# Performance work log

Measured on AMD Instinct MI355X. Metric: run time of the kernel, lower is better.

Reference implementation:

```python
import jax, jax.numpy as jnp
import numpy as np
from jax import lax

# ---- static config (from BasePllay_2 / AdTopoLayer(out_features=50, T=25, m0=0.2, lims=[[224,0],[0,224]], K_max=2, p=0)) ----
H = W = 28
G = H * W
T = 25
K_MAX = 2
M0 = 0.2
OUT_FEATURES = 50
B = 32
TSEQ = jnp.linspace(0.0, 100.0, T)  # fixed landscape sample grid (covers DTM value range)

# static grid geometry from lims=[[224,0],[0,224]]
_xs = np.linspace(224.0, 0.0, H)
_ys = np.linspace(0.0, 224.0, W)
_pts = np.stack(np.meshgrid(_xs, _ys, indexing="ij"), -1).reshape(G, 2)
_d = np.sqrt(((_pts[:, None] - _pts[None]) ** 2).sum(-1))
_sidx = np.argsort(_d, axis=-1)
SDIST = jnp.asarray(np.take_along_axis(_d, _sidx, -1), jnp.float32)  # [G,G] sorted distances per grid point
SIDX = jnp.asarray(_sidx.astype(np.int32))                            # [G,G] static distance-sort order

# 4-connectivity neighbor table for the cubical (pixel) grid, -1 = invalid
_ii = np.arange(G).reshape(H, W)
_nb = np.full((H, W, 4), -1, np.int32)
_nb[1:, :, 0] = _ii[:-1, :]
_nb[:-1, :, 1] = _ii[1:, :]
_nb[:, 1:, 2] = _ii[:, :-1]
_nb[:, :-1, 3] = _ii[:, 1:]
NBR = jnp.asarray(_nb.reshape(G, 4))


def dtm(w):
    """Weighted distance-to-measure (r=2) on the fixed grid. w: [B,G] nonneg -> [B,G]."""
    sw = w[:, SIDX]                               # [B,G,G] weights in distance order
    cw = jnp.cumsum(sw, -1)
    d2 = SDIST ** 2
    cwd = jnp.cumsum(sw * d2[None], -1)
    bound = M0 * w.sum(-1)                        # [B]
    k = jnp.argmax(cw >= bound[:, None, None], -1)  # [B,G] first index reaching mass bound
    km1 = jnp.maximum(k - 1, 0)
    take = lambda a, i: jnp.take_along_axis(a, i[..., None], -1)[..., 0]
    has_prev = k > 0
    cw_p = jnp.where(has_prev, take(cw, km1), 0.0)
    cwd_p = jnp.where(has_prev, take(cwd, km1), 0.0)
    dk2 = d2[jnp.arange(G)[None, :], k]           # [B,G]
    val = (cwd_p + (bound[:, None] - cw_p) * dk2) / bound[:, None]
    return jnp.sqrt(jnp.maximum(val, 0.0))


def pd0(vals):
    """0-dim sublevel-set persistence of vals on the pixel grid (union-find, elder rule).
    Returns (births[G], deaths[G]); non-merging pixels yield zero-persistence pairs,
    essential components die at the max filtration value."""
    order = jnp.argsort(vals).astype(jnp.int32)
    rank = jnp.zeros(G, jnp.int32).at[order].set(jnp.arange(G, dtype=jnp.int32))

    def find(parent, i):
        return lax.while_loop(lambda j: parent[j] != j, lambda j: parent[j], i)

    def step(s, carry):
        parent, death = carry
        p = order[s]
        best = p
        for t in range(4):  # unrolled over the 4 grid neighbors (static)
            q = NBR[p, t]
            ok = (q >= 0) & (rank[jnp.maximum(q, 0)] < s)  # neighbor already inserted
            r = find(parent, jnp.where(ok, q, p))
            merge = ok & (r != best)
            r_old = rank[r] < rank[best]
            older = jnp.where(r_old, r, best)
            younger = jnp.where(r_old, best, r)
            widx = jnp.where(merge, younger, G)   # slot G is a dummy
            parent = parent.at[widx].set(older)
            death = death.at[widx].set(p)         # younger component dies at pixel p
            best = jnp.where(merge, older, best)
        return parent, death

    parent0 = jnp.arange(G + 1, dtype=jnp.int32)
    death0 = jnp.full(G + 1, -1, jnp.int32)
    _, death = lax.fori_loop(0, G, step, (parent0, death0))
    d = death[:G]
    deaths = jnp.where(d >= 0, vals[jnp.maximum(d, 0)], vals.max())
    return vals, deaths


def landscape(births, deaths):
    """K_MAX persistence landscapes sampled at TSEQ. [B,G] -> [B, K_MAX*T]."""
    tb = TSEQ[None, :, None] - births[:, None, :]   # [B,T,G]
    td = deaths[:, None, :] - TSEQ[None, :, None]
    tent = jnp.maximum(jnp.minimum(tb, td), 0.0)
    topk = lax.top_k(tent, K_MAX)[0]                # [B,T,K]
    return jnp.transpose(topk, (0, 2, 1)).reshape(births.shape[0], K_MAX * T)


def _forward(x, w_land, b_land, w_fc, b_fc):
    w = x.reshape(x.shape[0], -1)          # nn.Flatten: pixel intensities as measure weights
    v = dtm(w)                             # [B,G]
    births, deaths = jax.vmap(pd0)(v)
    feats = landscape(births, deaths)      # [B, 50]
    xt = feats @ w_land.T + b_land         # AdTopoLayer output [B, out_features]
    signal = jnp.abs(lax.stop_gradient(xt)).sum(0)   # torch: x.detach().abs().sum(0)
    out = jnp.maximum(xt, 0.0) @ w_fc.T + b_fc       # fc(relu(x))
    return out, signal

_forward_jit = jax.jit(_forward)


def setup_inputs() -> dict:
    key = jax.random.key(0)
    k = jax.random.split(key, 4)
    x = jax.random.uniform(k[0], (B, 1, H, W), jnp.float32)  # image-like nonneg weights
    w_land = jax.random.normal(k[1], (OUT_FEATURES, K_MAX * T), jnp.float32) * 0.1
    b_land = jnp.zeros((OUT_FEATURES,), jnp.float32)
    w_fc = jax.random.normal(k[2], (10, OUT_FEATURES), jnp.float32) * 0.1
    b_fc = jnp.zeros((10,), jnp.float32)
    return {"x": x, "w_land": w_land, "b_land": b_land, "w_fc": w_fc, "b_fc": b_fc}


def reference(x, w_land, b_land, w_fc, b_fc):
    return _forward_jit(x, w_land, b_land, w_fc, b_fc)
```

## Files before the change

### kernel.cpp

```cpp
#include <hip/hip_runtime.h>
#include <math.h>

#define H28 28
#define G784 784
#define BATCH 32
#define NOFF 3025
#define NOFFP 3072
#define NKEY 1459
#define TPTS 25
#define KMAX 2
#define NFEAT 50
#define OUTF 50
#define NCLS 10

#define NBX 28
#define BT 512
#define BT2 512
#define HS 2048
#define EMAX 1024

struct OffPair { unsigned ij; float d2; };
struct OffTab  { OffPair e[NOFFP]; };

constexpr double csqrt(double x) {
  double r = x * 0.5 + 1.0;
  for (int i = 0; i < 20; i++) r = 0.5 * (r + x / r);
  return r;
}

constexpr OffTab make_offtab() {
  OffTab t{};
  int start[NKEY] = {};
  for (int i = 0; i < NOFF; i++) {
    int di = i / 55 - 27, dj = i % 55 - 27;
    start[di * di + dj * dj]++;
  }
  int run = 0;
  for (int k = 0; k < NKEY; k++) { int h = start[k]; start[k] = run; run += h; }
  for (int i = 0; i < NOFF; i++) {
    int di = i / 55 - 27, dj = i % 55 - 27;
    int key = di * di + dj * dj;
    int pos = start[key]++;
    float sd = (key == 0) ? 0.0f : (float)(csqrt((double)key) * (224.0 / 27.0));
    t.e[pos].ij = ((unsigned)(di & 0xffff)) | (((unsigned)(dj & 0xffff)) << 16);
    t.e[pos].d2 = sd * sd;
  }
  for (int i = NOFF; i < NOFFP; i++) { t.e[i].ij = 0x00640064u; t.e[i].d2 = 0.f; }
  return t;
}

__device__ constexpr OffTab OFFTAB = make_offtab();

__device__ __forceinline__ float wave_iscan_f32(float x) {
  int t;
  t = __builtin_amdgcn_update_dpp(0, __float_as_int(x), 0x111, 0xf, 0xf, true);
  x += __int_as_float(t);
  t = __builtin_amdgcn_update_dpp(0, __float_as_int(x), 0x112, 0xf, 0xf, true);
  x += __int_as_float(t);
  t = __builtin_amdgcn_update_dpp(0, __float_as_int(x), 0x114, 0xf, 0xf, true);
  x += __int_as_float(t);
  t = __builtin_amdgcn_update_dpp(0, __float_as_int(x), 0x118, 0xf, 0xf, true);
  x += __int_as_float(t);
  t = __builtin_amdgcn_update_dpp(0, __float_as_int(x), 0x142, 0xa, 0xf, true);
  x += __int_as_float(t);
  t = __builtin_amdgcn_update_dpp(0, __float_as_int(x), 0x143, 0xc, 0xf, true);
  x += __int_as_float(t);
  return x;
}

__global__ __launch_bounds__(BT) void dtm_kernel(const float* __restrict__ x,
                                                 float* __restrict__ v,
                                                 int* __restrict__ done_ctr) {
  __shared__ float w_s[G784];
  __shared__ float red[BT / 64];

  const int tid  = threadIdx.x;
  const int b    = blockIdx.x;
  const int bx   = blockIdx.y;
  const int wave = tid >> 6;
  const int lane = tid & 63;

  if (b == 0 && bx == 0 && tid == 0) *done_ctr = 0;

  float ps = 0.f;
  for (int i = tid; i < G784; i += BT) {
    float wv = x[b * G784 + i];
    w_s[i] = wv;
    ps += wv;
  }
  for (int off = 32; off > 0; off >>= 1) ps += __shfl_xor(ps, off);
  if (lane == 0) red[wave] = ps;
  __syncthreads();
  float tot = 0.f;
  for (int k = 0; k < BT / 64; k++) tot += red[k];
  const float bound = 0.2f * tot;

  const int slot = bx * 8 + wave;

  for (int g = slot; g < G784; g += NBX * 8) {
    const int i1 = g / H28, j1 = g % H28;
    float cw = 0.f, cwd = 0.f;
    float cwp = 0.f, cwdp = 0.f, dk2 = 0.f;
    bool crossed = false;
    int o = lane;
    unsigned ij = OFFTAB.e[o].ij;
    float d2v   = OFFTAB.e[o].d2;
    for (int base = 0; base < NOFFP && !crossed; base += 64) {
      int onext = o + 64;
      if (onext >= NOFFP) onext = o;
      const unsigned ij_n = OFFTAB.e[onext].ij;
      const float    d2_n = OFFTAB.e[onext].d2;
      const int di = (short)(ij & 0xffffu);
      const int dj = (short)(ij >> 16);
      const int i2 = i1 + di, j2 = j1 + dj;
      const bool inb = ((unsigned)i2 < (unsigned)H28) & ((unsigned)j2 < (unsigned)H28);
      const float wv = inb ? w_s[i2 * H28 + j2] : 0.f;
      const float wd = wv * d2v;
      const float psw = wave_iscan_f32(wv);
      const float psd = wave_iscan_f32(wd);
      const unsigned long long mask = __ballot(cw + psw >= bound);
      if (mask) {
        const int f = __ffsll((unsigned long long)mask) - 1;
        const float psw_f = __shfl(psw, f);
        const float w_f   = __shfl(wv, f);
        const float psd_f = __shfl(psd, f);
        const float wd_f  = __shfl(wd, f);
        dk2  = __shfl(d2v, f);
        cwp  = cw + (psw_f - w_f);
        cwdp = cwd + (psd_f - wd_f);
        crossed = true;
      } else {
        cw  += __int_as_float(__builtin_amdgcn_readlane(__float_as_int(psw), 63));
        cwd += __int_as_float(__builtin_amdgcn_readlane(__float_as_int(psd), 63));
      }
      ij = ij_n; d2v = d2_n; o = onext;
    }
    const float val = (cwdp + (bound - cwp) * dk2) / bound;
    if (lane == 0) v[b * G784 + g] = sqrtf(fmaxf(val, 0.f));
  }
}

__device__ __forceinline__ unsigned long long pix_key(const float* val_s, int p) {
  return (((unsigned long long)__float_as_uint(val_s[p])) << 10) | (unsigned)p;
}

__global__ __launch_bounds__(BT2) void pd0_kernel(const float* __restrict__ v,
                                                  float* __restrict__ feats,
                                                  int* __restrict__ done_ctr,
                                                  const float* __restrict__ w_land,
                                                  const float* __restrict__ b_land,
                                                  const float* __restrict__ w_fc,
                                                  const float* __restrict__ b_fc,
                                                  float* __restrict__ out) {
  __shared__ float val_s[G784];
  __shared__ int   ptr_s[G784];
  __shared__ int   parent[G784];
  __shared__ unsigned rank_s[G784];
  __shared__ unsigned claims[G784];
  __shared__ float deathv[G784];
  __shared__ int   mlist[G784];
  __shared__ unsigned long long oldkey[G784];
  __shared__ unsigned htag[HS];
  __shared__ unsigned long long hval[HS];
  __shared__ unsigned long long edges[EMAX];
  __shared__ float redf[BT2 / 64];
  __shared__ int   mcnt_sh, ecnt_sh, last_sh;
  __shared__ float xt_s[BATCH * OUTF];

  const int tid  = threadIdx.x;
  const int b    = blockIdx.x;
  const int wave = tid >> 6;
  const int lane = tid & 63;
  if (tid == 0) { mcnt_sh = 0; ecnt_sh = 0; }

  for (int i = tid; i < HS; i += BT2) { htag[i] = 0u; hval[i] = ~0ULL; }

  float pm = -1e30f;
  for (int i = tid; i < G784; i += BT2) {
    float xv = v[b * G784 + i];
    val_s[i] = xv;
    pm = fmaxf(pm, xv);
    rank_s[i] = 0u;
    claims[i] = 0xFFFFFFFFu;
  }
  for (int off = 32; off > 0; off >>= 1) pm = fmaxf(pm, __shfl_xor(pm, off));
  if (lane == 0) redf[wave] = pm;
  __syncthreads();
  float vmax = redf[0];
  for (int k = 1; k < BT2 / 64; k++) vmax = fmaxf(vmax, redf[k]);

  for (int p = tid; p < G784; p += BT2) {
    unsigned long long kp = pix_key(val_s, p);
    int i = p / H28, j = p % H28;
    int nbs[4];
    nbs[0] = (i > 0)       ? p - H28 : -1;
    nbs[1] = (i < H28 - 1) ? p + H28 : -1;
    nbs[2] = (j > 0)       ? p - 1   : -1;
    nbs[3] = (j < H28 - 1) ? p + 1   : -1;
    int best = p;
    unsigned long long bk = kp;
    for (int t = 0; t < 4; t++) {
      int q = nbs[t];
      if (q >= 0) {
        unsigned long long kq = pix_key(val_s, q);
        if (kq < bk) { bk = kq; best = q; }
      }
    }
    ptr_s[p]  = best;
    parent[p] = p;
    deathv[p] = vmax;
    if (best == p) {
      oldkey[p] = kp;
      int mi = atomicAdd(&mcnt_sh, 1);
      mlist[mi] = p;
    }
  }
  __syncthreads();

  for (int r = 0; r < 10; r++) {
    for (int p = tid; p < G784; p += BT2) ptr_s[p] = ptr_s[ptr_s[p]];
    __syncthreads();
  }

  for (int p = tid; p < G784; p += BT2) {
    unsigned long long kp = pix_key(val_s, p);
    int i = p / H28, j = p % H28;
    int nbs[4];
    nbs[0] = (i > 0)       ? p - H28 : -1;
    nbs[1] = (i < H28 - 1) ? p + H28 : -1;
    nbs[2] = (j > 0)       ? p - 1   : -1;
    nbs[3] = (j < H28 - 1) ? p + 1   : -1;
    int bp = ptr_s[p];
    for (int t = 0; t < 4; t++) {
      int q = nbs[t];
      if (q >= 0) {
        unsigned long long kq = pix_key(val_s, q);
        int bq = ptr_s[q];
        if (kq < kp && bq != bp) {
          unsigned long long key =
              (((unsigned long long)__float_as_uint(val_s[p])) << 32) |
              (((unsigned long long)(unsigned)p) << 22) |
              (((unsigned long long)(unsigned)t) << 20) |
              (((unsigned long long)(unsigned)bp) << 10) |
              ((unsigned long long)(unsigned)bq);
          unsigned lo = (bp < bq) ? (unsigned)bp : (unsigned)bq;
          unsigned hi = (bp < bq) ? (unsigned)bq : (unsigned)bp;
          unsigned pairid = (lo << 10) | hi;
          unsigned idx = (pairid * 2654435761u) >> 21;
          for (;;) {
            unsigned t0 = atomicCAS(&htag[idx], 0u, pairid + 1u);
            if (t0 == 0u || t0 == pairid + 1u) { atomicMin(&hval[idx], key); break; }
            idx = (idx + 1) & (HS - 1);
          }
        }
      }
    }
  }
  __syncthreads();

  for (int i = tid; i < HS; i += BT2) {
    if (htag[i]) {
      int e = atomicAdd(&ecnt_sh, 1);
      if (e < EMAX) edges[e] = hval[i];
    }
  }
  __syncthreads();
  const int ne   = (ecnt_sh < EMAX) ? ecnt_sh : EMAX;
  const int mcnt = mcnt_sh;

  {
    unsigned long long m0 = 0, m1 = 0;
    int r0 = 0, r1 = 0;
    const int i0 = tid, i1 = tid + BT2;
    const bool h0 = (i0 < ne), h1 = (i1 < ne);
    if (h0) m0 = edges[i0];
    if (h1) m1 = edges[i1];
    for (int j = 0; j < ne; j++) {
      unsigned long long ej = edges[j];
      r0 += (ej < m0) ? 1 : 0;
      r1 += (ej < m1) ? 1 : 0;
    }
    if (h0) hval[r0] = m0;
    if (h1) hval[r1] = m1;
  }
  __syncthreads();
  const unsigned long long* sedges = hval;

  if (wave == 0) {
    int merged = 0;
    const int target = mcnt - 1;
    for (int base = 0; base < ne && merged < target; base += 64) {
      const int idx = base + lane;
      bool unresolved = (idx < ne);
      const unsigned long long e = unresolved ? sedges[idx] : 0ULL;
      const int A  = (int)((e >> 10) & 1023u);
      const int Bq = (int)(e & 1023u);
      const float ev = __uint_as_float((unsigned)(e >> 32));
      for (;;) {
        int rA = A, rB = Bq;
        if (unresolved) {
          int xx = A;
          for (;;) { int p1 = parent[xx]; if (p1 == xx) break;
                     int p2 = parent[p1]; parent[xx] = p2; xx = p2; }
          rA = xx;
          xx = Bq;
          for (;;) { int p1 = parent[xx]; if (p1 == xx) break;
                     int p2 = parent[p1]; parent[xx] = p2; xx = p2; }
          rB = xx;
        }
        bool crossing = unresolved && (rA != rB);
        if (unresolved && !crossing) unresolved = false;
        if (__ballot(crossing) == 0ULL) break;
        if (crossing) {
          atomicMin(&claims[rA], (unsigned)lane);
          atomicMin(&claims[rB], (unsigned)lane);
        }
        __threadfence_block();
        bool win = crossing && claims[rA] == (unsigned)lane
                            && claims[rB] == (unsigned)lane;
        __threadfence_block();
        if (crossing) { claims[rA] = 0xFFFFFFFFu; claims[rB] = 0xFFFFFFFFu; }
        if (win) {
          unsigned long long ka = oldkey[rA], kb = oldkey[rB];
          unsigned ra_ = rank_s[rA], rb_ = rank_s[rB];
          int big   = (ra_ > rb_) ? rA : ((rb_ > ra_) ? rB : ((rA < rB) ? rA : rB));
          int small = (big == rA) ? rB : rA;
          parent[small] = big;
          if (ra_ == rb_) rank_s[big] = ra_ + 1u;
          unsigned long long okmin = (ka < kb) ? ka : kb;
          unsigned long long okmax = (ka < kb) ? kb : ka;
          oldkey[big] = okmin;
          int dying = (int)(okmax & 1023u);
          deathv[dying] = ev;
          unresolved = false;
        }
        __threadfence_block();
        merged += (int)__popcll(__ballot(win));
        if (merged >= target) break;
      }
    }
    __threadfence_block();

    if (lane < TPTS) {
      float ti = (float)((double)lane * (100.0 / 24.0));
      float t1 = 0.f, t2 = 0.f;
      for (int ii = 0; ii < mcnt; ii++) {
        int m = mlist[ii];
        float tent = fminf(ti - val_s[m], deathv[m] - ti);
        tent = fmaxf(tent, 0.f);
        if (tent > t1)      { t2 = t1; t1 = tent; }
        else if (tent > t2) { t2 = tent; }
      }
      feats[b * NFEAT + lane]        = t1;
      feats[b * NFEAT + TPTS + lane] = t2;
    }
  }

  __threadfence();
  __syncthreads();
  if (tid == 0) last_sh = (atomicAdd(done_ctr, 1) == BATCH - 1) ? 1 : 0;
  __syncthreads();
  if (!last_sh) return;
  __threadfence();

  for (int idx = tid; idx < BATCH * OUTF; idx += BT2) {
    int bb = idx / OUTF, ff = idx % OUTF;
    float acc = b_land[ff];
    const float* wr = w_land + ff * NFEAT;
    const float* fr = feats + bb * NFEAT;
    for (int j = 0; j < NFEAT; j++) acc += fr[j] * wr[j];
    xt_s[idx] = acc;
  }
  __syncthreads();
  if (tid < OUTF) {
    float s = 0.f;
    for (int bb = 0; bb < BATCH; bb++) s += fabsf(xt_s[bb * OUTF + tid]);
    out[BATCH * NCLS + tid] = s;
  }
  for (int idx = tid; idx < BATCH * NCLS; idx += BT2) {
    int bb = idx / NCLS, cc = idx % NCLS;
    float acc = b_fc[cc];
    const float* wr = w_fc + cc * OUTF;
    const float* xr = xt_s + bb * OUTF;
    for (int ff = 0; ff < OUTF; ff++) acc += fmaxf(xr[ff], 0.f) * wr[ff];
    out[bb * NCLS + cc] = acc;
  }
}

extern "C" void kernel_launch(void* const* d_in, const int* in_sizes, int n_in,
                              void* d_out, int out_size, void* d_ws, size_t ws_size,
                              hipStream_t stream) {
  (void)in_sizes; (void)n_in; (void)out_size; (void)ws_size;
  const float* x      = (const float*)d_in[0];
  const float* w_land = (const float*)d_in[1];
  const float* b_land = (const float*)d_in[2];
  const float* w_fc   = (const float*)d_in[3];
  const float* b_fc   = (const float*)d_in[4];
  float* out   = (float*)d_out;
  float* v     = (float*)d_ws;
  float* feats = v + BATCH * G784;
  int*   done  = (int*)(feats + BATCH * NFEAT);

  dim3 g1(BATCH, NBX);
  dtm_kernel<<<g1, BT, 0, stream>>>(x, v, done);
  pd0_kernel<<<BATCH, BT2, 0, stream>>>(v, feats, done,
                                        w_land, b_land, w_fc, b_fc, out);
}
```

Baseline: 102.7 us.

## Parallelize landscape top-2 across waves and replace fixed pointer jumping with chain walk

```diff
diff --git a/kernel.cpp b/kernel.cpp
--- a/kernel.cpp
+++ b/kernel.cpp
@@ -18,6 +18,8 @@
 #define BT2 512
 #define HS 2048
 #define EMAX 1024
+
+typedef unsigned long long u64;
 
 struct OffPair { unsigned ij; float d2; };
 struct OffTab  { OffPair e[NOFFP]; };
@@ -118,9 +120,9 @@
       const float wd = wv * d2v;
       const float psw = wave_iscan_f32(wv);
       const float psd = wave_iscan_f32(wd);
-      const unsigned long long mask = __ballot(cw + psw >= bound);
+      const u64 mask = __ballot(cw + psw >= bound);
       if (mask) {
-        const int f = __ffsll((unsigned long long)mask) - 1;
+        const int f = __ffsll((u64)mask) - 1;
         const float psw_f = __shfl(psw, f);
         const float w_f   = __shfl(wv, f);
         const float psd_f = __shfl(psd, f);
@@ -140,8 +142,8 @@
   }
 }
 
-__device__ __forceinline__ unsigned long long pix_key(const float* val_s, int p) {
-  return (((unsigned long long)__float_as_uint(val_s[p])) << 10) | (unsigned)p;
+__device__ __forceinline__ u64 pix_key(const float* val_s, int p) {
+  return (((u64)__float_as_uint(val_s[p])) << 10) | (unsigned)p;
 }
 
 __global__ __launch_bounds__(BT2) void pd0_kernel(const float* __restrict__ v,
@@ -159,11 +161,13 @@
   __shared__ unsigned claims[G784];
   __shared__ float deathv[G784];
   __shared__ int   mlist[G784];
-  __shared__ unsigned long long oldkey[G784];
+  __shared__ u64   oldkey[G784];
   __shared__ unsigned htag[HS];
-  __shared__ unsigned long long hval[HS];
-  __shared__ unsigned long long edges[EMAX];
+  __shared__ u64   hval[HS];
+  __shared__ u64   edges[EMAX];
   __shared__ float redf[BT2 / 64];
+  __shared__ float lt1[8][32];
+  __shared__ float lt2[8][32];
   __shared__ int   mcnt_sh, ecnt_sh, last_sh;
   __shared__ float xt_s[BATCH * OUTF];
 
@@ -172,58 +176,63 @@
   const int wave = tid >> 6;
   const int lane = tid & 63;
   if (tid == 0) { mcnt_sh = 0; ecnt_sh = 0; }
-
+  __syncthreads();
+
+  const float* vb = v + b * G784;
+  float pm = -1e30f;
+  for (int p = tid; p < G784; p += BT2) {
+    int i = p / H28, j = p % H28;
+    float vp = vb[p];
+    val_s[p] = vp;
+    pm = fmaxf(pm, vp);
+    u64 bk = (((u64)__float_as_uint(vp)) << 10) | (unsigned)p;
+    int best = p;
+    if (i > 0) {
+      int q = p - H28; u64 kq = (((u64)__float_as_uint(vb[q])) << 10) | (unsigned)q;
+      if (kq < bk) { bk = kq; best = q; }
+    }
+    if (i < H28 - 1) {
+      int q = p + H28; u64 kq = (((u64)__float_as_uint(vb[q])) << 10) | (unsigned)q;
+      if (kq < bk) { bk = kq; best = q; }
+    }
+    if (j > 0) {
+      int q = p - 1; u64 kq = (((u64)__float_as_uint(vb[q])) << 10) | (unsigned)q;
+      if (kq < bk) { bk = kq; best = q; }
+    }
+    if (j < H28 - 1) {
+      int q = p + 1; u64 kq = (((u64)__float_as_uint(vb[q])) << 10) | (unsigned)q;
+      if (kq < bk) { bk = kq; best = q; }
+    }
+    ptr_s[p] = best;
+    if (best == p) { int mi = atomicAdd(&mcnt_sh, 1); mlist[mi] = p; }
+  }
   for (int i = tid; i < HS; i += BT2) { htag[i] = 0u; hval[i] = ~0ULL; }
-
-  float pm = -1e30f;
-  for (int i = tid; i < G784; i += BT2) {
-    float xv = v[b * G784 + i];
-    val_s[i] = xv;
-    pm = fmaxf(pm, xv);
-    rank_s[i] = 0u;
-    claims[i] = 0xFFFFFFFFu;
-  }
   for (int off = 32; off > 0; off >>= 1) pm = fmaxf(pm, __shfl_xor(pm, off));
   if (lane == 0) redf[wave] = pm;
   __syncthreads();
+
   float vmax = redf[0];
   for (int k = 1; k < BT2 / 64; k++) vmax = fmaxf(vmax, redf[k]);
+  const int mcnt = mcnt_sh;
 
   for (int p = tid; p < G784; p += BT2) {
-    unsigned long long kp = pix_key(val_s, p);
-    int i = p / H28, j = p % H28;
-    int nbs[4];
-    nbs[0] = (i > 0)       ? p - H28 : -1;
-    nbs[1] = (i < H28 - 1) ? p + H28 : -1;
-    nbs[2] = (j > 0)       ? p - 1   : -1;
-    nbs[3] = (j < H28 - 1) ? p + 1   : -1;
-    int best = p;
-    unsigned long long bk = kp;
-    for (int t = 0; t < 4; t++) {
-      int q = nbs[t];
-      if (q >= 0) {
-        unsigned long long kq = pix_key(val_s, q);
-        if (kq < bk) { bk = kq; best = q; }
-      }
-    }
-    ptr_s[p]  = best;
-    parent[p] = p;
-    deathv[p] = vmax;
-    if (best == p) {
-      oldkey[p] = kp;
-      int mi = atomicAdd(&mcnt_sh, 1);
-      mlist[mi] = p;
-    }
-  }
-  __syncthreads();
-
-  for (int r = 0; r < 10; r++) {
-    for (int p = tid; p < G784; p += BT2) ptr_s[p] = ptr_s[ptr_s[p]];
-    __syncthreads();
-  }
+    int x = ptr_s[p];
+    int y = ptr_s[x];
+    while (y != x) { x = y; y = ptr_s[x]; }
+    ptr_s[p] = x;
+  }
+  for (int i = tid; i < mcnt; i += BT2) {
+    int m = mlist[i];
+    parent[m] = m;
+    rank_s[m] = 0u;
+    claims[m] = 0xFFFFFFFFu;
+    deathv[m] = vmax;
+    oldkey[m] = pix_key(val_s, m);
+  }
+  __syncthreads();
 
   for (int p = tid; p < G784; p += BT2) {
-    unsigned long long kp = pix_key(val_s, p);
+    u64 kp = pix_key(val_s, p);
     int i = p / H28, j = p % H28;
     int nbs[4];
     nbs[0] = (i > 0)       ? p - H28 : -1;
@@ -234,15 +243,14 @@
     for (int t = 0; t < 4; t++) {
       int q = nbs[t];
       if (q >= 0) {
-        unsigned long long kq = pix_key(val_s, q);
+        u64 kq = pix_key(val_s, q);
         int bq = ptr_s[q];
         if (kq < kp && bq != bp) {
-          unsigned long long key =
-              (((unsigned long long)__float_as_uint(val_s[p])) << 32) |
-              (((unsigned long long)(unsigned)p) << 22) |
-              (((unsigned long long)(unsigned)t) << 20) |
-              (((unsigned long long)(unsigned)bp) << 10) |
-              ((unsigned long long)(unsigned)bq);
+          u64 key = (((u64)__float_as_uint(val_s[p])) << 32) |
+                    (((u64)(unsigned)p) << 22) |
+                    (((u64)(unsigned)t) << 20) |
+                    (((u64)(unsigned)bp) << 10) |
+                    ((u64)(unsigned)bq);
           unsigned lo = (bp < bq) ? (unsigned)bp : (unsigned)bq;
           unsigned hi = (bp < bq) ? (unsigned)bq : (unsigned)bp;
           unsigned pairid = (lo << 10) | hi;
@@ -265,18 +273,17 @@
     }
   }
   __syncthreads();
-  const int ne   = (ecnt_sh < EMAX) ? ecnt_sh : EMAX;
-  const int mcnt = mcnt_sh;
+  const int ne = (ecnt_sh < EMAX) ? ecnt_sh : EMAX;
 
   {
-    unsigned long long m0 = 0, m1 = 0;
+    u64 m0 = 0, m1 = 0;
     int r0 = 0, r1 = 0;
     const int i0 = tid, i1 = tid + BT2;
     const bool h0 = (i0 < ne), h1 = (i1 < ne);
     if (h0) m0 = edges[i0];
     if (h1) m1 = edges[i1];
     for (int j = 0; j < ne; j++) {
-      unsigned long long ej = edges[j];
+      u64 ej = edges[j];
       r0 += (ej < m0) ? 1 : 0;
       r1 += (ej < m1) ? 1 : 0;
     }
@@ -284,7 +291,7 @@
     if (h1) hval[r1] = m1;
   }
   __syncthreads();
-  const unsigned long long* sedges = hval;
+  const u64* sedges = hval;
 
   if (wave == 0) {
     int merged = 0;
@@ -292,7 +299,7 @@
     for (int base = 0; base < ne && merged < target; base += 64) {
       const int idx = base + lane;
       bool unresolved = (idx < ne);
-      const unsigned long long e = unresolved ? sedges[idx] : 0ULL;
+      const u64 e = unresolved ? sedges[idx] : 0ULL;
       const int A  = (int)((e >> 10) & 1023u);
       const int Bq = (int)(e & 1023u);
       const float ev = __uint_as_float((unsigned)(e >> 32));
@@ -321,14 +328,14 @@
         __threadfence_block();
         if (crossing) { claims[rA] = 0xFFFFFFFFu; claims[rB] = 0xFFFFFFFFu; }
         if (win) {
-          unsigned long long ka = oldkey[rA], kb = oldkey[rB];
+          u64 ka = oldkey[rA], kb = oldkey[rB];
           unsigned ra_ = rank_s[rA], rb_ = rank_s[rB];
           int big   = (ra_ > rb_) ? rA : ((rb_ > ra_) ? rB : ((rA < rB) ? rA : rB));
           int small = (big == rA) ? rB : rA;
           parent[small] = big;
           if (ra_ == rb_) rank_s[big] = ra_ + 1u;
-          unsigned long long okmin = (ka < kb) ? ka : kb;
-          unsigned long long okmax = (ka < kb) ? kb : ka;
+          u64 okmin = (ka < kb) ? ka : kb;
+          u64 okmax = (ka < kb) ? kb : ka;
           oldkey[big] = okmin;
           int dying = (int)(okmax & 1023u);
           deathv[dying] = ev;
@@ -339,21 +346,34 @@
         if (merged >= target) break;
       }
     }
-    __threadfence_block();
-
-    if (lane < TPTS) {
-      float ti = (float)((double)lane * (100.0 / 24.0));
-      float t1 = 0.f, t2 = 0.f;
-      for (int ii = 0; ii < mcnt; ii++) {
-        int m = mlist[ii];
-        float tent = fminf(ti - val_s[m], deathv[m] - ti);
-        tent = fmaxf(tent, 0.f);
-        if (tent > t1)      { t2 = t1; t1 = tent; }
-        else if (tent > t2) { t2 = tent; }
-      }
-      feats[b * NFEAT + lane]        = t1;
-      feats[b * NFEAT + TPTS + lane] = t2;
-    }
+  }
+  __syncthreads();
+
+  {
+    float ti = (lane < TPTS) ? (float)((double)lane * (100.0 / 24.0)) : 0.f;
+    float t1 = 0.f, t2 = 0.f;
+    for (int ii = wave; ii < mcnt; ii += 8) {
+      int m = mlist[ii];
+      float birth = val_s[m];
+      float death = deathv[m];
+      float tent = fmaxf(fminf(ti - birth, death - ti), 0.f);
+      if (tent > t1)      { t2 = t1; t1 = tent; }
+      else if (tent > t2) { t2 = tent; }
+    }
+    if (lane < TPTS) { lt1[wave][lane] = t1; lt2[wave][lane] = t2; }
+  }
+  __syncthreads();
+
+  if (wave == 0 && lane < TPTS) {
+    float t1 = 0.f, t2 = 0.f;
+    for (int w = 0; w < 8; w++) {
+      float a1 = lt1[w][lane], a2 = lt2[w][lane];
+      float nt1 = fmaxf(t1, a1);
+      float nt2 = fmaxf(fminf(t1, a1), fmaxf(t2, a2));
+      t1 = nt1; t2 = nt2;
+    }
+    feats[b * NFEAT + lane]        = t1;
+    feats[b * NFEAT + TPTS + lane] = t2;
   }
 
   __threadfence();
```

Result: no change. 102.1 us (-0.6%).
